# Performance work log

Measured on AMD Instinct MI355X. Metric: run time of the kernel, lower is better.

Reference implementation:

```python
import jax, jax.numpy as jnp
import numpy as np

N_HEADS = 16
N_KV_HEADS = 4
HEAD_DIM = 128  # n_embd // n_head = 2048 // 16
NEG_INF = -1e9


def setup_inputs() -> dict:
    key = jax.random.key(0)
    ks = jax.random.split(key, 4)
    B, T, C = 8, 1024, 2048
    x = jax.random.normal(ks[0], (B, T, C), dtype=jnp.float32)
    sc = 1.0 / np.sqrt(C)
    Wq = jax.random.normal(ks[1], (C, C), dtype=jnp.float32) * sc
    bq = jnp.zeros((C,), dtype=jnp.float32)
    Wkv = jax.random.normal(ks[2], (N_KV_HEADS * HEAD_DIM * 2, C), dtype=jnp.float32) * sc
    bkv = jnp.zeros((N_KV_HEADS * HEAD_DIM * 2,), dtype=jnp.float32)
    Wo = jax.random.normal(ks[3], (C, C), dtype=jnp.float32) * sc
    bo = jnp.zeros((C,), dtype=jnp.float32)
    return {"x": x, "Wq": Wq, "bq": bq, "Wkv": Wkv, "bkv": bkv, "Wo": Wo, "bo": bo}


def reference(x, Wq, bq, Wkv, bkv, Wo, bo):
    B, T, C = x.shape
    g = N_HEADS // N_KV_HEADS  # group size for repeat_interleave
    # q: [B, H, T, D]
    q = (x @ Wq.T + bq).reshape(B, T, N_HEADS, HEAD_DIM).transpose(0, 2, 1, 3)
    # kv: [B, T, Hkv, 2, D] -> [B, Hkv, T, 2, D]
    kv = (x @ Wkv.T + bkv).reshape(B, T, N_KV_HEADS, 2, HEAD_DIM).transpose(0, 2, 1, 3, 4)
    k = kv[..., 0, :]  # [B, Hkv, T, D]
    v = kv[..., 1, :]
    # repeat_interleave along head dim to expand kv heads to full heads
    k = jnp.repeat(k, g, axis=1)  # [B, H, T, D]
    v = jnp.repeat(v, g, axis=1)
    scale = 1.0 / jnp.sqrt(jnp.asarray(HEAD_DIM, dtype=x.dtype))
    scores = jnp.einsum('bhqd,bhkd->bhqk', q, k) * scale  # [B, H, T, T]
    causal = jnp.tril(jnp.ones((T, T), dtype=bool))
    scores = jnp.where(causal[None, None], scores, NEG_INF)
    attn = jax.nn.softmax(scores, axis=-1)
    y = jnp.einsum('bhqk,bhkd->bhqd', attn, v)  # [B, H, T, D]
    y = y.transpose(0, 2, 1, 3).reshape(B, T, C)
    return y @ Wo.T + bo
```

## Files before the change

kernel.cpp:

```cpp
#include <hip/hip_runtime.h>

typedef short short8 __attribute__((ext_vector_type(8)));
typedef short short4v __attribute__((ext_vector_type(4)));
typedef float floatx4 __attribute__((ext_vector_type(4)));
typedef unsigned short ushort_t;
typedef unsigned int uint_t;

#define DI __device__ __forceinline__

DI ushort_t f2bf(float f) {
  uint_t u = __builtin_bit_cast(uint_t, f);
  uint_t r = u + 0x7FFFu + ((u >> 16) & 1u);
  return (ushort_t)(r >> 16);
}

DI float exp2a(float x) {
  float r;
  asm("v_exp_f32 %0, %1" : "=v"(r) : "v"(x));
  return r;
}

DI floatx4 mfma16(short8 a, short8 b, floatx4 c) {
  return __builtin_amdgcn_mfma_f32_16x16x32_bf16(a, b, c, 0, 0, 0);
}

DI void async16(const void* g, void* l) {
  __builtin_amdgcn_global_load_lds(
      (__attribute__((address_space(1))) void*)(g),
      (__attribute__((address_space(3))) void*)(l), 16, 0, 0);
}

DI void cfence() { asm volatile("" ::: "memory"); }

__global__ __launch_bounds__(256)
void k_f2bf4(const float* __restrict__ x, const float* __restrict__ wq,
             const float* __restrict__ wkv, const float* __restrict__ wo,
             ushort_t* __restrict__ xb, ushort_t* __restrict__ wqb,
             ushort_t* __restrict__ wkvb, ushort_t* __restrict__ wob)
{
  const int blk = blockIdx.x;
  const float* in; ushort_t* out; long base;
  if (blk < 8192)       { in = x;   out = xb;   base = (long)blk * 2048; }
  else if (blk < 10240) { in = wq;  out = wqb;  base = (long)(blk - 8192) * 2048; }
  else if (blk < 11264) { in = wkv; out = wkvb; base = (long)(blk - 10240) * 2048; }
  else                  { in = wo;  out = wob;  base = (long)(blk - 11264) * 2048; }
  const long i = base + (long)threadIdx.x * 8;
  const float4 a = *(const float4*)(in + i);
  const float4 b = *(const float4*)(in + i + 4);
  union { short8 s; ushort_t u[8]; } o;
  o.u[0] = f2bf(a.x); o.u[1] = f2bf(a.y); o.u[2] = f2bf(a.z); o.u[3] = f2bf(a.w);
  o.u[4] = f2bf(b.x); o.u[5] = f2bf(b.y); o.u[6] = f2bf(b.z); o.u[7] = f2bf(b.w);
  *(short8*)(out + i) = o.s;
}

__global__ __launch_bounds__(256)
void k_gemmkv(const ushort_t* __restrict__ A, const ushort_t* __restrict__ B,
              const float* __restrict__ bias, ushort_t* __restrict__ KVout,
              ushort_t* __restrict__ Vt, int N, int K)
{
  __shared__ __align__(16) ushort_t As[4][128 * 32];
  __shared__ __align__(16) ushort_t Bs[4][128 * 32];
  const int tid = threadIdx.x;
  const int w = tid >> 6, l = tid & 63;
  const int wm = w >> 1, wn = w & 1;
  const int lr = l & 15, lg = l >> 4;
  const long m0 = (long)blockIdx.y * 128;
  const long n0 = (long)blockIdx.x * 128;

  const floatx4 fz = {0.f, 0.f, 0.f, 0.f};
  floatx4 acc[4][4];
#pragma unroll
  for (int i = 0; i < 4; ++i)
#pragma unroll
    for (int j = 0; j < 4; ++j) acc[i][j] = fz;

  const int c0 = tid, c1 = 256 + tid;
  const int r0 = c0 >> 2, r1 = c1 >> 2;
  const ushort_t* gA0 = A + (m0 + r0) * K + (((c0 & 3) ^ (r0 & 3)) << 3);
  const ushort_t* gA1 = A + (m0 + r1) * K + (((c1 & 3) ^ (r1 & 3)) << 3);
  const ushort_t* gB0 = B + (n0 + r0) * K + (((c0 & 3) ^ (r0 & 3)) << 3);
  const ushort_t* gB1 = B + (n0 + r1) * K + (((c1 & 3) ^ (r1 & 3)) << 3);

  const int nK = K >> 5;
#pragma unroll
  for (int pt = 0; pt < 3; ++pt) {
    const int ko = pt << 5;
    async16(gA0 + ko, &As[pt][c0 * 8]);
    async16(gA1 + ko, &As[pt][c1 * 8]);
    async16(gB0 + ko, &Bs[pt][c0 * 8]);
    async16(gB1 + ko, &Bs[pt][c1 * 8]);
  }

  const int xg = (lr & 3);

  for (int kt = 0; kt < nK; ++kt) {
    const int cur = kt & 3;
    const int rem = nK - 1 - kt;
    if (rem >= 3) {
      const int ko = (kt + 3) << 5;
      const int nb = (kt + 3) & 3;
      async16(gA0 + ko, &As[nb][c0 * 8]);
      async16(gA1 + ko, &As[nb][c1 * 8]);
      async16(gB0 + ko, &Bs[nb][c0 * 8]);
      async16(gB1 + ko, &Bs[nb][c1 * 8]);
      asm volatile("s_waitcnt vmcnt(12)" ::: "memory");
    } else if (rem == 2) {
      asm volatile("s_waitcnt vmcnt(8)" ::: "memory");
    } else if (rem == 1) {
      asm volatile("s_waitcnt vmcnt(4)" ::: "memory");
    } else {
      asm volatile("s_waitcnt vmcnt(0)" ::: "memory");
    }
    __builtin_amdgcn_s_barrier();
    cfence();

    short8 a[4], b[4];
#pragma unroll
    for (int i = 0; i < 4; ++i)
      a[i] = *(const short8*)&As[cur][(wm * 64 + i * 16 + lr) * 32 + ((lg ^ xg) * 8)];
#pragma unroll
    for (int j = 0; j < 4; ++j)
      b[j] = *(const short8*)&Bs[cur][(wn * 64 + j * 16 + lr) * 32 + ((lg ^ xg) * 8)];
#pragma unroll
    for (int i = 0; i < 4; ++i)
#pragma unroll
      for (int j = 0; j < 4; ++j)
        acc[i][j] = mfma16(a[i], b[j], acc[i][j]);

    asm volatile("s_waitcnt lgkmcnt(0)" ::: "memory");
    __builtin_amdgcn_s_barrier();
    cfence();
  }

#pragma unroll
  for (int j = 0; j < 4; ++j) {
    const long gn = n0 + wn * 64 + j * 16 + lr;
    const float bv = bias[gn];
    const int isV = (int)((gn >> 7) & 1);
    const long vrowB = (long)((gn >> 8) * 128 + (gn & 127)) * 1024;
#pragma unroll
    for (int i = 0; i < 4; ++i) {
      const long gm = m0 + wm * 64 + i * 16 + lg * 4;
#pragma unroll
      for (int r = 0; r < 4; ++r) {
        const ushort_t ov = f2bf(acc[i][j][r] + bv);
        const long gmr = gm + r;
        if (isV) Vt[((gmr >> 10) * 512) * 1024 + vrowB + (gmr & 1023)] = ov;
        else     KVout[gmr * 1024 + gn] = ov;
      }
    }
  }
}

#define STG_A2(t_, h_, bf_) do { \
    async16(aS + (h_)*128*K + (t_)*64,        &Al[bf_][(h_)*8192 + dD]); \
    async16(aS + ((h_)*128+64)*K + (t_)*64,   &Al[bf_][(h_)*8192 + 4096 + dD]); } while(0)
#define STG_B2(t_, h_, bf_) do { \
    async16(bS + (h_)*128*K + (t_)*64,        &Bl[bf_][(h_)*8192 + dD]); \
    async16(bS + ((h_)*128+64)*K + (t_)*64,   &Bl[bf_][(h_)*8192 + 4096 + dD]); } while(0)
#define LDA2(bf_, mh_) { _Pragma("unroll") for (int i = 0; i < 4; ++i) { \
    aA[i] = *(const short8*)&Al[bf_][raB + ((mh_)*4+i)*1024 + g0]; \
    aB[i] = *(const short8*)&Al[bf_][raB + ((mh_)*4+i)*1024 + g1]; } }
#define LDB2_0(bf_) { _Pragma("unroll") for (int j = 0; j < 2; ++j) { \
    bA0[j] = *(const short8*)&Bl[bf_][rbB + j*1024 + g0]; \
    bB0[j] = *(const short8*)&Bl[bf_][rbB + j*1024 + g1]; } }
#define LDB2_1(bf_) { _Pragma("unroll") for (int j = 0; j < 2; ++j) { \
    bA1[j] = *(const short8*)&Bl[bf_][rbB + (2+j)*1024 + g0]; \
    bB1[j] = *(const short8*)&Bl[bf_][rbB + (2+j)*1024 + g1]; } }
#define MFQ2(mh_, nh_, bA_, bB_) { _Pragma("unroll") for (int i = 0; i < 4; ++i) \
    _Pragma("unroll") for (int j = 0; j < 2; ++j) { \
      acc[(mh_)*4+i][(nh_)*2+j] = mfma16(aA[i], bA_[j], acc[(mh_)*4+i][(nh_)*2+j]); \
      acc[(mh_)*4+i][(nh_)*2+j] = mfma16(aB[i], bB_[j], acc[(mh_)*4+i][(nh_)*2+j]); } }
#define WAITV2(n_) asm volatile("s_waitcnt vmcnt(" #n_ ")" ::: "memory")
#define BARC      { __builtin_amdgcn_s_barrier(); cfence(); }
#define PRIO1     __builtin_amdgcn_s_setprio(1)
#define PRIO0     __builtin_amdgcn_s_setprio(0)

template<int OUT_BF16>
__global__ __launch_bounds__(512, 2)
void k_gemm2(const ushort_t* __restrict__ A, const ushort_t* __restrict__ B,
             const float* __restrict__ bias, void* __restrict__ Cout,
             int N, int K, int gx, float out_scale)
{
  __shared__ __align__(16) ushort_t Al[2][256 * 64];
  __shared__ __align__(16) ushort_t Bl[2][256 * 64];
  const int tid = threadIdx.x;
  const int w = tid >> 6, l = tid & 63;
  const int wr = w >> 2, wc = w & 3;
  const int lr = l & 15, lg = l >> 4;

  const int nwg = gridDim.x;
  const int qd = nwg >> 3;
  const int p = blockIdx.x;
  const int swz = (p & 7) * qd + (p >> 3);
  const long m0 = (long)(swz / gx) * 256;
  const long n0 = (long)(swz % gx) * 256;

  const floatx4 fz = {0.f, 0.f, 0.f, 0.f};
  floatx4 acc[8][4];
#pragma unroll
  for (int i = 0; i < 8; ++i)
#pragma unroll
    for (int j = 0; j < 4; ++j) acc[i][j] = fz;

  const int rowL = tid >> 3, s = tid & 7;
  const int sx = s ^ (rowL & 7);
  const ushort_t* aS = A + (m0 + rowL) * K + sx * 8;
  const ushort_t* bS = B + (n0 + rowL) * K + sx * 8;
  const int dD = rowL * 64 + s * 8;

  const int raB = (wr * 128 + lr) * 64;
  const int rbB = (wc * 64 + lr) * 64;
  const int x8 = lr & 7;
  const int g0 = (lg ^ x8) * 8;
  const int g1 = ((4 + lg) ^ x8) * 8;

  short8 aA[4], aB[4], bA0[2], bB0[2], bA1[2], bB1[2];

  const int nT = K >> 6;
  STG_A2(0, 0, 0);
  STG_B2(0, 0, 0);
  STG_B2(0, 1, 0);
  STG_A2(0, 1, 0);
  WAITV2(4); BARC;

  for (int t = 0; t < nT - 1; ++t) {
    const int cur = t & 1, nxt = cur ^ 1;
    LDA2(cur, 0); LDB2_0(cur);
    STG_A2(t + 1, 0, nxt);
    BARC;
    PRIO1; MFQ2(0, 0, bA0, bB0); PRIO0;
    WAITV2(4); BARC;
    LDB2_1(cur);
    STG_B2(t + 1, 0, nxt);
    BARC;
    PRIO1; MFQ2(0, 1, bA1, bB1); PRIO0;
    WAITV2(4); BARC;
    LDA2(cur, 1);
    STG_B2(t + 1, 1, nxt);
    BARC;
    PRIO1; MFQ2(1, 1, bA1, bB1); PRIO0;
    BARC;
    STG_A2(t + 1, 1, nxt);
    PRIO1; MFQ2(1, 0, bA0, bB0); PRIO0;
    WAITV2(4); BARC;
  }
  {
    const int cur = (nT - 1) & 1;
    LDA2(cur, 0); LDB2_0(cur);
    PRIO1; MFQ2(0, 0, bA0, bB0); PRIO0;
    WAITV2(2); BARC;
    LDB2_1(cur);
    PRIO1; MFQ2(0, 1, bA1, bB1); PRIO0;
    WAITV2(0); BARC;
    LDA2(cur, 1);
    PRIO1; MFQ2(1, 1, bA1, bB1); MFQ2(1, 0, bA0, bB0); PRIO0;
  }

#pragma unroll
  for (int j = 0; j < 4; ++j) {
    const long gn = n0 + wc * 64 + j * 16 + lr;
    const float bv = bias[gn];
#pragma unroll
    for (int i = 0; i < 8; ++i) {
      const long gm = m0 + wr * 128 + i * 16 + lg * 4;
#pragma unroll
      for (int r = 0; r < 4; ++r) {
        const float v = (acc[i][j][r] + bv) * out_scale;
        if (OUT_BF16) ((ushort_t*)Cout)[(gm + r) * N + gn] = f2bf(v);
        else          ((float*)Cout)[(gm + r) * N + gn] = v;
      }
    }
  }
}

__global__ __launch_bounds__(256)
void k_attn(const ushort_t* __restrict__ Q, const ushort_t* __restrict__ KV,
            const ushort_t* __restrict__ Vt, ushort_t* __restrict__ Y)
{
  __shared__ __align__(16) ushort_t Kl[2][64 * 128];
  __shared__ __align__(16) ushort_t Vl[2][128 * 64];
  __shared__ __align__(16) ushort_t Pl[4][16][72];
  const int tid = threadIdx.x;
  const int w = tid >> 6, l = tid & 63;
  const int lr = l & 15, lg = l >> 4;
  const int p = blockIdx.x;
  const int v = ((p & 7) << 8) | (p >> 3);
  const int b = v >> 8;
  const int kh = (v >> 6) & 3;
  const int hs = (v >> 4) & 3;
  const int qt = 15 - (v & 15);
  const int h = kh * 4 + hs;
  const int qrow = qt * 64 + w * 16;

  const ushort_t* qptr = Q + ((long)(b * 1024 + qrow + lr)) * 2048 + h * 128 + lg * 8;
  short8 qf[4];
#pragma unroll
  for (int c = 0; c < 4; ++c) qf[c] = *(const short8*)(qptr + c * 32);

  const ushort_t* kg[4];
  const ushort_t* vg[4];
  int ld[4];
#pragma unroll
  for (int i = 0; i < 4; ++i) {
    const int c = i * 256 + tid;
    const int row = c >> 4, sgk = (c & 15) ^ (row & 7);
    kg[i] = KV + ((long)(b * 1024 + row)) * 1024 + kh * 256 + sgk * 8;
    const int d = c >> 3, sgv = (c & 7) ^ (d & 7);
    vg[i] = Vt + ((long)((b * 4 + kh) * 128 + d)) * 1024 + sgv * 8;
    ld[i] = c * 8;
  }

  float m_s = 0.f;
  float l_p = 0.f;
  const floatx4 fz = {0.f, 0.f, 0.f, 0.f};
  floatx4 yacc[8];
#pragma unroll
  for (int dt = 0; dt < 8; ++dt) yacc[dt] = fz;

  const int xk = (lr & 7) << 4;

#pragma unroll
  for (int i = 0; i < 4; ++i) async16(kg[i], &Kl[0][ld[i]]);
#pragma unroll
  for (int i = 0; i < 4; ++i) async16(vg[i], &Vl[0][ld[i]]);

  for (int t = 0; t <= qt; ++t) {
    const ushort_t* KlC = &Kl[t & 1][0];
    const ushort_t* VlC = &Vl[t & 1][0];
    asm volatile("s_waitcnt vmcnt(0)" ::: "memory");
    asm volatile("s_waitcnt lgkmcnt(0)" ::: "memory");
    __builtin_amdgcn_s_barrier();
    cfence();
    if (t < qt) {
      const long ko = (long)(t + 1) * 65536;
      const long vo = (long)(t + 1) * 64;
      ushort_t* KlN = &Kl[(t + 1) & 1][0];
      ushort_t* VlN = &Vl[(t + 1) & 1][0];
#pragma unroll
      for (int i = 0; i < 4; ++i) async16(kg[i] + ko, &KlN[ld[i]]);
#pragma unroll
      for (int i = 0; i < 4; ++i) async16(vg[i] + vo, &VlN[ld[i]]);
    }

    const floatx4 finit = {-m_s, -m_s, -m_s, -m_s};
    floatx4 st[4];
#pragma unroll
    for (int k2 = 0; k2 < 4; ++k2) {
      floatx4 sacc = finit;
      const int row = k2 * 16 + lr;
#pragma unroll
      for (int c = 0; c < 4; ++c) {
        const int off = row * 256 + ((c * 64 + lg * 16) ^ xk);
        const short8 kf = *(const short8*)((const char*)KlC + off);
        sacc = mfma16(kf, qf[c], sacc);
      }
      st[k2] = sacc;
    }
    if (t == qt) {
      const int qg = qrow + lr;
#pragma unroll
      for (int k2 = 0; k2 < 4; ++k2)
#pragma unroll
        for (int r = 0; r < 4; ++r)
          if (t * 64 + k2 * 16 + lg * 4 + r > qg) st[k2][r] = -__builtin_inff();
    }
    float pm = -__builtin_inff();
#pragma unroll
    for (int k2 = 0; k2 < 4; ++k2)
      pm = fmaxf(pm, fmaxf(fmaxf(st[k2][0], st[k2][1]), fmaxf(st[k2][2], st[k2][3])));
    if (!__all(pm <= 8.f)) {
      float pmf = fmaxf(pm, __shfl_xor(pm, 16));
      pmf = fmaxf(pmf, __shfl_xor(pmf, 32));
      const float d = fmaxf(pmf, 0.f);
      m_s += d;
      const float corr = exp2a(-d);
      l_p *= corr;
      const float cc0 = __shfl(corr, lg * 4 + 0);
      const float cc1 = __shfl(corr, lg * 4 + 1);
      const float cc2 = __shfl(corr, lg * 4 + 2);
      const float cc3 = __shfl(corr, lg * 4 + 3);
#pragma unroll
      for (int dt = 0; dt < 8; ++dt) {
        yacc[dt][0] *= cc0; yacc[dt][1] *= cc1;
        yacc[dt][2] *= cc2; yacc[dt][3] *= cc3;
      }
#pragma unroll
      for (int k2 = 0; k2 < 4; ++k2)
#pragma unroll
        for (int r = 0; r < 4; ++r) st[k2][r] -= d;
    }
    float psum = 0.f;
#pragma unroll
    for (int k2 = 0; k2 < 4; ++k2) {
      const float pe0 = exp2a(st[k2][0]);
      const float pe1 = exp2a(st[k2][1]);
      const float pe2 = exp2a(st[k2][2]);
      const float pe3 = exp2a(st[k2][3]);
      psum += (pe0 + pe1) + (pe2 + pe3);
      uint_t d0, d1;
      asm("v_cvt_pk_bf16_f32 %0, %1, %2" : "=v"(d0) : "v"(pe0), "v"(pe1));
      asm("v_cvt_pk_bf16_f32 %0, %1, %2" : "=v"(d1) : "v"(pe2), "v"(pe3));
      uint2 pkv; pkv.x = d0; pkv.y = d1;
      *(uint2*)&Pl[w][lr][k2 * 16 + lg * 4] = pkv;
    }
    l_p += psum;
    asm volatile("s_waitcnt lgkmcnt(0)" ::: "memory");

#pragma unroll
    for (int kc = 0; kc < 2; ++kc) {
      const short8 pf = *(const short8*)&Pl[w][lr][kc * 32 + lg * 8];
#pragma unroll
      for (int dt = 0; dt < 8; ++dt) {
        const int d = dt * 16 + lr;
        const int off = d * 128 + ((kc * 64 + lg * 16) ^ xk);
        const short8 vf = *(const short8*)((const char*)VlC + off);
        yacc[dt] = mfma16(pf, vf, yacc[dt]);
      }
    }
    cfence();
  }

  float l_s = l_p;
  l_s += __shfl_xor(l_s, 16);
  l_s += __shfl_xor(l_s, 32);
  const float linv = 1.f / l_s;
  const float i0 = __shfl(linv, lg * 4 + 0);
  const float i1 = __shfl(linv, lg * 4 + 1);
  const float i2 = __shfl(linv, lg * 4 + 2);
  const float i3 = __shfl(linv, lg * 4 + 3);
  ushort_t* yp = Y + ((long)(b * 1024 + qrow)) * 2048 + h * 128 + lr;
#pragma unroll
  for (int dt = 0; dt < 8; ++dt) {
    yp[(long)(lg * 4 + 0) * 2048 + dt * 16] = f2bf(yacc[dt][0] * i0);
    yp[(long)(lg * 4 + 1) * 2048 + dt * 16] = f2bf(yacc[dt][1] * i1);
    yp[(long)(lg * 4 + 2) * 2048 + dt * 16] = f2bf(yacc[dt][2] * i2);
    yp[(long)(lg * 4 + 3) * 2048 + dt * 16] = f2bf(yacc[dt][3] * i3);
  }
}

extern "C" void kernel_launch(void* const* d_in, const int* in_sizes, int n_in,
                              void* d_out, int out_size, void* d_ws, size_t ws_size,
                              hipStream_t stream)
{
  (void)in_sizes; (void)n_in; (void)out_size;
  const float* x   = (const float*)d_in[0];
  const float* Wq  = (const float*)d_in[1];
  const float* bq  = (const float*)d_in[2];
  const float* Wkv = (const float*)d_in[3];
  const float* bkv = (const float*)d_in[4];
  const float* Wo  = (const float*)d_in[5];
  const float* bo  = (const float*)d_in[6];
  float* out = (float*)d_out;
  char* ws = (char*)d_ws;

  if (ws_size < 104857600) return;

  ushort_t* xb   = (ushort_t*)(ws);
  ushort_t* Qb   = (ushort_t*)(ws + 33554432);
  ushort_t* KVb  = (ushort_t*)(ws + 67108864);
  ushort_t* Wqb  = (ushort_t*)(ws + 83886080);
  ushort_t* Wkvb = (ushort_t*)(ws + 92274688);
  ushort_t* Wob  = (ushort_t*)(ws + 96468992);
  ushort_t* Vtb  = Wqb;
  ushort_t* Yb   = xb;

  k_f2bf4<<<dim3(13312), 256, 0, stream>>>(x, Wq, Wkv, Wo, xb, Wqb, Wkvb, Wob);

  const float scale = 0.12751743f;
  k_gemm2<1><<<dim3(256), 512, 0, stream>>>(xb, Wqb, bq, Qb, 2048, 2048, 8, scale);
  k_gemmkv<<<dim3(8, 64), 256, 0, stream>>>(xb, Wkvb, bkv, KVb, Vtb, 1024, 2048);
  k_attn<<<dim3(2048), 256, 0, stream>>>(Qb, KVb, Vtb, Yb);
  k_gemm2<0><<<dim3(256), 512, 0, stream>>>(Yb, Wob, bo, out, 2048, 2048, 8, 1.0f);
}
```

Before: 307.8 us.

## Replace 256x256 GEMM with simpler 256x128 tile, K=32 double-buffered kernel

Swaps the heavily interleaved 256x256 K64 projection GEMM for a smaller 256x128 tile with a K-step of 32 and a simple double-buffered loop: one wait and barrier per step, then loads and 16 MFMAs per wave. The grid doubles to 512 workgroups, and launch bounds now allow 4 blocks per CU for higher occupancy. The trade-off is lower arithmetic intensity per tile, more global traffic, and a full vmcnt(0) wait each step, which exposes load latency that the old schedule overlapped with compute.

```diff
diff --git a/kernel.cpp b/kernel.cpp
--- a/kernel.cpp
+++ b/kernel.cpp
@@ -152,41 +152,17 @@
   }
 }
 
-#define STG_A2(t_, h_, bf_) do { \
-    async16(aS + (h_)*128*K + (t_)*64,        &Al[bf_][(h_)*8192 + dD]); \
-    async16(aS + ((h_)*128+64)*K + (t_)*64,   &Al[bf_][(h_)*8192 + 4096 + dD]); } while(0)
-#define STG_B2(t_, h_, bf_) do { \
-    async16(bS + (h_)*128*K + (t_)*64,        &Bl[bf_][(h_)*8192 + dD]); \
-    async16(bS + ((h_)*128+64)*K + (t_)*64,   &Bl[bf_][(h_)*8192 + 4096 + dD]); } while(0)
-#define LDA2(bf_, mh_) { _Pragma("unroll") for (int i = 0; i < 4; ++i) { \
-    aA[i] = *(const short8*)&Al[bf_][raB + ((mh_)*4+i)*1024 + g0]; \
-    aB[i] = *(const short8*)&Al[bf_][raB + ((mh_)*4+i)*1024 + g1]; } }
-#define LDB2_0(bf_) { _Pragma("unroll") for (int j = 0; j < 2; ++j) { \
-    bA0[j] = *(const short8*)&Bl[bf_][rbB + j*1024 + g0]; \
-    bB0[j] = *(const short8*)&Bl[bf_][rbB + j*1024 + g1]; } }
-#define LDB2_1(bf_) { _Pragma("unroll") for (int j = 0; j < 2; ++j) { \
-    bA1[j] = *(const short8*)&Bl[bf_][rbB + (2+j)*1024 + g0]; \
-    bB1[j] = *(const short8*)&Bl[bf_][rbB + (2+j)*1024 + g1]; } }
-#define MFQ2(mh_, nh_, bA_, bB_) { _Pragma("unroll") for (int i = 0; i < 4; ++i) \
-    _Pragma("unroll") for (int j = 0; j < 2; ++j) { \
-      acc[(mh_)*4+i][(nh_)*2+j] = mfma16(aA[i], bA_[j], acc[(mh_)*4+i][(nh_)*2+j]); \
-      acc[(mh_)*4+i][(nh_)*2+j] = mfma16(aB[i], bB_[j], acc[(mh_)*4+i][(nh_)*2+j]); } }
-#define WAITV2(n_) asm volatile("s_waitcnt vmcnt(" #n_ ")" ::: "memory")
-#define BARC      { __builtin_amdgcn_s_barrier(); cfence(); }
-#define PRIO1     __builtin_amdgcn_s_setprio(1)
-#define PRIO0     __builtin_amdgcn_s_setprio(0)
-
 template<int OUT_BF16>
-__global__ __launch_bounds__(512, 2)
-void k_gemm2(const ushort_t* __restrict__ A, const ushort_t* __restrict__ B,
+__global__ __launch_bounds__(512, 4)
+void k_gemm3(const ushort_t* __restrict__ A, const ushort_t* __restrict__ B,
              const float* __restrict__ bias, void* __restrict__ Cout,
              int N, int K, int gx, float out_scale)
 {
-  __shared__ __align__(16) ushort_t Al[2][256 * 64];
-  __shared__ __align__(16) ushort_t Bl[2][256 * 64];
+  __shared__ __align__(16) ushort_t Al[2][256 * 32];
+  __shared__ __align__(16) ushort_t Bl[2][128 * 32];
   const int tid = threadIdx.x;
   const int w = tid >> 6, l = tid & 63;
-  const int wr = w >> 2, wc = w & 3;
+  const int wr = w >> 1, wc = w & 1;
   const int lr = l & 15, lg = l >> 4;
 
   const int nwg = gridDim.x;
@@ -194,67 +170,58 @@
   const int p = blockIdx.x;
   const int swz = (p & 7) * qd + (p >> 3);
   const long m0 = (long)(swz / gx) * 256;
-  const long n0 = (long)(swz % gx) * 256;
+  const long n0 = (long)(swz % gx) * 128;
 
   const floatx4 fz = {0.f, 0.f, 0.f, 0.f};
-  floatx4 acc[8][4];
-#pragma unroll
-  for (int i = 0; i < 8; ++i)
+  floatx4 acc[4][4];
+#pragma unroll
+  for (int i = 0; i < 4; ++i)
 #pragma unroll
     for (int j = 0; j < 4; ++j) acc[i][j] = fz;
 
-  const int rowL = tid >> 3, s = tid & 7;
-  const int sx = s ^ (rowL & 7);
-  const ushort_t* aS = A + (m0 + rowL) * K + sx * 8;
-  const ushort_t* bS = B + (n0 + rowL) * K + sx * 8;
-  const int dD = rowL * 64 + s * 8;
-
-  const int raB = (wr * 128 + lr) * 64;
-  const int rbB = (wc * 64 + lr) * 64;
-  const int x8 = lr & 7;
-  const int g0 = (lg ^ x8) * 8;
-  const int g1 = ((4 + lg) ^ x8) * 8;
-
-  short8 aA[4], aB[4], bA0[2], bB0[2], bA1[2], bB1[2];
-
-  const int nT = K >> 6;
-  STG_A2(0, 0, 0);
-  STG_B2(0, 0, 0);
-  STG_B2(0, 1, 0);
-  STG_A2(0, 1, 0);
-  WAITV2(4); BARC;
-
-  for (int t = 0; t < nT - 1; ++t) {
-    const int cur = t & 1, nxt = cur ^ 1;
-    LDA2(cur, 0); LDB2_0(cur);
-    STG_A2(t + 1, 0, nxt);
-    BARC;
-    PRIO1; MFQ2(0, 0, bA0, bB0); PRIO0;
-    WAITV2(4); BARC;
-    LDB2_1(cur);
-    STG_B2(t + 1, 0, nxt);
-    BARC;
-    PRIO1; MFQ2(0, 1, bA1, bB1); PRIO0;
-    WAITV2(4); BARC;
-    LDA2(cur, 1);
-    STG_B2(t + 1, 1, nxt);
-    BARC;
-    PRIO1; MFQ2(1, 1, bA1, bB1); PRIO0;
-    BARC;
-    STG_A2(t + 1, 1, nxt);
-    PRIO1; MFQ2(1, 0, bA0, bB0); PRIO0;
-    WAITV2(4); BARC;
-  }
-  {
-    const int cur = (nT - 1) & 1;
-    LDA2(cur, 0); LDB2_0(cur);
-    PRIO1; MFQ2(0, 0, bA0, bB0); PRIO0;
-    WAITV2(2); BARC;
-    LDB2_1(cur);
-    PRIO1; MFQ2(0, 1, bA1, bB1); PRIO0;
-    WAITV2(0); BARC;
-    LDA2(cur, 1);
-    PRIO1; MFQ2(1, 1, bA1, bB1); MFQ2(1, 0, bA0, bB0); PRIO0;
+  const int cA0 = tid, cA1 = 512 + tid, cB = tid;
+  const int rA0 = cA0 >> 2, rA1 = cA1 >> 2, rB = cB >> 2;
+  const ushort_t* aS0 = A + (m0 + rA0) * K + (((cA0 & 3) ^ (rA0 & 3)) << 3);
+  const ushort_t* aS1 = A + (m0 + rA1) * K + (((cA1 & 3) ^ (rA1 & 3)) << 3);
+  const ushort_t* bS  = B + (n0 + rB) * K + (((cB & 3) ^ (rB & 3)) << 3);
+  const int dA0 = cA0 * 8, dA1 = cA1 * 8, dB = cB * 8;
+
+  const int xs = lg ^ (lr & 3);
+  const int raB = (wr * 64 + lr) * 32 + xs * 8;
+  const int rbB = (wc * 64 + lr) * 32 + xs * 8;
+
+  const int nT = K >> 5;
+  async16(aS0, &Al[0][dA0]);
+  async16(aS1, &Al[0][dA1]);
+  async16(bS,  &Bl[0][dB]);
+
+  for (int t = 0; t < nT; ++t) {
+    const int cur = t & 1;
+    asm volatile("s_waitcnt vmcnt(0)" ::: "memory");
+    asm volatile("s_waitcnt lgkmcnt(0)" ::: "memory");
+    __builtin_amdgcn_s_barrier();
+    cfence();
+    if (t + 1 < nT) {
+      const int ko = (t + 1) << 5;
+      async16(aS0 + ko, &Al[cur ^ 1][dA0]);
+      async16(aS1 + ko, &Al[cur ^ 1][dA1]);
+      async16(bS + ko,  &Bl[cur ^ 1][dB]);
+    }
+    short8 a[4], b[4];
+#pragma unroll
+    for (int i = 0; i < 4; ++i)
+      a[i] = *(const short8*)&Al[cur][raB + i * 512];
+#pragma unroll
+    for (int j = 0; j < 4; ++j)
+      b[j] = *(const short8*)&Bl[cur][rbB + j * 512];
+    __builtin_amdgcn_s_setprio(1);
+#pragma unroll
+    for (int i = 0; i < 4; ++i)
+#pragma unroll
+      for (int j = 0; j < 4; ++j)
+        acc[i][j] = mfma16(a[i], b[j], acc[i][j]);
+    __builtin_amdgcn_s_setprio(0);
+    cfence();
   }
 
 #pragma unroll
@@ -262,8 +229,8 @@
     const long gn = n0 + wc * 64 + j * 16 + lr;
     const float bv = bias[gn];
 #pragma unroll
-    for (int i = 0; i < 8; ++i) {
-      const long gm = m0 + wr * 128 + i * 16 + lg * 4;
+    for (int i = 0; i < 4; ++i) {
+      const long gm = m0 + wr * 64 + i * 16 + lg * 4;
 #pragma unroll
       for (int r = 0; r < 4; ++r) {
         const float v = (acc[i][j][r] + bv) * out_scale;
@@ -468,8 +435,8 @@
   k_f2bf4<<<dim3(13312), 256, 0, stream>>>(x, Wq, Wkv, Wo, xb, Wqb, Wkvb, Wob);
 
   const float scale = 0.12751743f;
-  k_gemm2<1><<<dim3(256), 512, 0, stream>>>(xb, Wqb, bq, Qb, 2048, 2048, 8, scale);
+  k_gemm3<1><<<dim3(512), 512, 0, stream>>>(xb, Wqb, bq, Qb, 2048, 2048, 16, scale);
   k_gemmkv<<<dim3(8, 64), 256, 0, stream>>>(xb, Wkvb, bkv, KVb, Vtb, 1024, 2048);
   k_attn<<<dim3(2048), 256, 0, stream>>>(Qb, KVb, Vtb, Yb);
-  k_gemm2<0><<<dim3(256), 512, 0, stream>>>(Yb, Wob, bo, out, 2048, 2048, 8, 1.0f);
-}
+  k_gemm3<0><<<dim3(512), 512, 0, stream>>>(Yb, Wob, bo, out, 2048, 2048, 16, 1.0f);
+}
```

Result: slower. 318.8 us (+3.6%).
